# Kernel optimization log

Measured on AMD Instinct MI355X. Metric: run time of the kernel, lower is better.

The kernel has to match this reference:

```python
import jax, jax.numpy as jnp
import numpy as np

TOPK = 15
SIGMA = 2.0
VAR = (0.1, 0.2)


def point_form(p):  # cxcywh -> xyxy
    return jnp.concatenate([p[..., :2] - p[..., 2:] / 2, p[..., :2] + p[..., 2:] / 2], -1)


def decode(loc, priors):  # loc [P,4], priors cxcywh [P,4] -> xyxy
    xy = priors[:, :2] + loc[:, :2] * VAR[0] * priors[:, 2:]
    wh = priors[:, 2:] * jnp.exp(loc[:, 2:] * VAR[1])
    return jnp.concatenate([xy - wh / 2, xy + wh / 2], -1)


def encode(matched, priors):  # matched xyxy [...,4], priors cxcywh [...,4]
    g_cxcy = ((matched[..., :2] + matched[..., 2:]) / 2 - priors[..., :2]) / (VAR[0] * priors[..., 2:])
    g_wh = jnp.log((matched[..., 2:] - matched[..., :2]) / priors[..., 2:]) / VAR[1]
    return jnp.concatenate([g_cxcy, g_wh], -1)


def jaccard(a, b):  # a [O,4], b [P,4] xyxy -> [O,P]
    lt = jnp.maximum(a[:, None, :2], b[None, :, :2])
    rb = jnp.minimum(a[:, None, 2:], b[None, :, 2:])
    wh = jnp.clip(rb - lt, 0.0)
    inter = wh[..., 0] * wh[..., 1]
    area_a = (a[:, 2] - a[:, 0]) * (a[:, 3] - a[:, 1])
    area_b = (b[:, 2] - b[:, 0]) * (b[:, 3] - b[:, 1])
    return inter / (area_a[:, None] + area_b[None, :] - inter)


def boost_topk(mat):
    # per object row: num_pos = max(1, int(sum of top-15 scores)); add 3.0 to top num_pos anchors
    vals, idxs = jax.lax.top_k(mat, TOPK)                       # [O,TOPK]
    num_pos = jnp.maximum(1, vals.sum(axis=1).astype(jnp.int32))  # trunc like .int()
    add = jnp.where(jnp.arange(TOPK)[None, :] < num_pos[:, None], 3.0, 0.0)
    return jax.vmap(lambda row, i, a: row.at[i].add(a))(mat, idxs, add)


def mutual_match(truths, labels, regress, classif, priors):
    reg_ov = jaccard(truths, decode(regress, priors))           # [O,P]
    reg_ov = jnp.where(reg_ov == reg_ov.max(0, keepdims=True), reg_ov, 0.0)
    reg_ov = boost_topk(reg_ov)
    overlap_t = reg_ov.max(0)
    conf_t = labels[jnp.argmax(reg_ov, 0)] + 1
    ov = jaccard(truths, point_form(priors))                    # [O,P]
    pc = jax.nn.sigmoid(classif)[:, labels].T                   # [O,P]
    pred = ov ** ((SIGMA - pc) / SIGMA)
    pred = jnp.where(pred == pred.max(0, keepdims=True), pred, 0.0)
    pred = boost_topk(pred)
    pred_t = pred.max(0)
    loc_t = truths[jnp.argmax(pred, 0)]
    return loc_t, conf_t, overlap_t, pred_t


def balanced_l1(pred, target, alpha=0.5, gamma=1.5, beta=0.11):
    diff = jnp.abs(pred - target)
    b = np.float32(np.e ** (gamma / alpha) - 1.0)
    small = alpha / b * (b * diff + 1.0) * jnp.log1p(b * diff / beta) - alpha * diff
    big = gamma * diff + gamma / b - alpha * beta
    return jnp.where(diff < beta, small, big)


def gfocal_loss(logits, targets, gamma=2.0):
    # quality focal loss with soft IoU targets
    bce = jnp.maximum(logits, 0.0) - logits * targets + jnp.log1p(jnp.exp(-jnp.abs(logits)))
    scale = jnp.abs(jax.nn.sigmoid(logits) - targets) ** gamma
    num_pos = jnp.maximum((targets > 0).sum().astype(logits.dtype), 1.0)
    return (scale * bce).sum() / num_pos


def setup_inputs() -> dict:
    key = jax.random.key(0)
    k1, k2, k3, k4, k5, k6 = jax.random.split(key, 6)
    N, P, C, O = 32, 18000, 80, 16
    loc_data = jax.random.normal(k1, (N, P, 4), jnp.float32)
    conf_data = jax.random.normal(k2, (N, P, C), jnp.float32)
    pc = jax.random.uniform(k3, (P, 2), minval=0.05, maxval=0.95)
    pwh = jax.random.uniform(k4, (P, 2), minval=0.02, maxval=0.3)
    priors = jnp.concatenate([pc, pwh], -1)                     # cxcywh
    tc = jax.random.uniform(k5, (N, O, 2), minval=0.2, maxval=0.8)
    twh = jax.random.uniform(jax.random.fold_in(k5, 1), (N, O, 2), minval=0.05, maxval=0.4)
    truths = jnp.clip(jnp.concatenate([tc - twh / 2, tc + twh / 2], -1), 0.0, 1.0)  # xyxy
    labels = jax.random.randint(k6, (N, O), 0, C)
    return {"loc_data": loc_data, "conf_data": conf_data, "priors": priors,
            "truths": truths, "labels": labels}


def reference(loc_data, conf_data, priors, truths, labels):
    loc_t, conf_t, overlap_t, pred_t = jax.vmap(
        lambda t, l, r, c: mutual_match(t, l, r, c, priors)
    )(truths, labels, loc_data, conf_data)
    loc_t = jax.lax.stop_gradient(loc_t)          # matching done under no_grad
    overlap_t = jax.lax.stop_gradient(overlap_t)
    pred_t = jax.lax.stop_gradient(pred_t)

    # localization: weighted balanced L1 over positives (pred_t >= 3 -> weight relu(pred_t-3))
    w = jnp.broadcast_to(jax.nn.relu(pred_t - 3.0)[..., None], loc_data.shape)
    w = w / w.sum()
    pri = jnp.broadcast_to(priors[None], loc_data.shape)
    target = jax.lax.stop_gradient(encode(loc_t, pri))
    loss_l = (balanced_l1(loc_data, target) * w).sum()

    # classification: soft one-hot targets weighted by relu(overlap_t-3)
    num_classes = conf_data.shape[-1]
    conf_tz = jnp.where(overlap_t <= 1.0, 0, conf_t)
    batch_label = jax.nn.one_hot(conf_tz, num_classes + 1, dtype=conf_data.dtype)[..., 1:]
    batch_label = batch_label * jax.nn.relu(overlap_t - 3.0)[..., None]
    batch_label = jax.lax.stop_gradient(batch_label)
    loss_c = gfocal_loss(conf_data, batch_label)
    return loss_l, loss_c
```

## Files before the change

### kernel.cpp

```cpp
#include <hip/hip_runtime.h>
#include <hip/hip_bf16.h>

typedef unsigned long long u64;
typedef unsigned int u32;

#define LOG2E 1.44269504088896340736f
#define LN2   0.69314718055994530942f
#define CAP   768

__device__ __forceinline__ float fexp2(float x) { return __builtin_amdgcn_exp2f(x); }
__device__ __forceinline__ float flog2(float x) { return __builtin_amdgcn_logf(x); }
__device__ __forceinline__ float frcp(float x)  { return __builtin_amdgcn_rcpf(x); }
__device__ __forceinline__ float keyval(u64 k) { return __uint_as_float((u32)(k >> 32)); }

__device__ __forceinline__ float iou_xyxy(float ax1, float ay1, float ax2, float ay2,
                                          float bx1, float by1, float bx2, float by2) {
    float ltx = fmaxf(ax1, bx1), lty = fmaxf(ay1, by1);
    float rbx = fminf(ax2, bx2), rby = fminf(ay2, by2);
    float w = fmaxf(rbx - ltx, 0.0f), h = fmaxf(rby - lty, 0.0f);
    float inter = w * h;
    float areaA = (ax2 - ax1) * (ay2 - ay1);
    float areaB = (bx2 - bx1) * (by2 - by1);
    return inter / (areaA + areaB - inter);
}

__global__ __launch_bounds__(256) void k_main(
        const float* __restrict__ loc, const float* __restrict__ conf,
        const float* __restrict__ priors, const float* __restrict__ truths,
        const int* __restrict__ labels,
        u64* __restrict__ basekeyR, u64* __restrict__ basekeyP,
        double* __restrict__ partC, u32* __restrict__ pcnt, u32* __restrict__ pcnt2,
        int P) {
    int n = blockIdx.y, p0 = blockIdx.x * 64, tid = threadIdx.x;
    int r = tid >> 2, sub = tid & 3, p = p0 + r;
    bool act = p < P;

    if (blockIdx.x == 0 && tid == 0) { pcnt[n] = 0u; pcnt2[n] = 0u; }

    float4 L0, L1, L2, L3, L4, prv, lc;
    L0 = L1 = L2 = L3 = L4 = prv = lc = make_float4(0.f, 0.f, 0.f, 0.f);
    if (act) {
        const float* rowp = conf + ((size_t)n * P + p) * 80 + sub * 4;
        L0 = *(const float4*)(rowp);
        L1 = *(const float4*)(rowp + 16);
        L2 = *(const float4*)(rowp + 32);
        L3 = *(const float4*)(rowp + 48);
        L4 = *(const float4*)(rowp + 64);
        prv = *(const float4*)(priors + (size_t)p * 4);
        lc  = *(const float4*)(loc + ((size_t)n * P + p) * 4);
    }

    __shared__ float strt[64];
    __shared__ int   lab[16];
    __shared__ u32   smask[80];
    __shared__ float sglab[64][17];
    if (tid < 64) strt[tid] = truths[n * 64 + tid];
    if (tid < 80) smask[tid] = 0u;
    __syncthreads();
    if (tid < 16) {
        int lb = labels[n * 16 + tid];
        lab[tid] = lb;
        atomicOr(&smask[lb], 1u << tid);
    }
    __syncthreads();

    u32 mybits = 0;
    #pragma unroll
    for (int k = 0; k < 5; k++) {
        #pragma unroll
        for (int j = 0; j < 4; j++) {
            if (smask[k * 16 + sub * 4 + j]) mybits |= 1u << (k * 4 + j);
        }
    }

    {
        float vv[4] = {0, 0, 0, 0};
        float vmax = 0.0f;
        if (act) {
            float cx = prv.x + lc.x * 0.1f * prv.z;
            float cy = prv.y + lc.y * 0.1f * prv.w;
            float w  = prv.z * fexp2(lc.z * 0.2f * LOG2E);
            float h  = prv.w * fexp2(lc.w * 0.2f * LOG2E);
            float bx1 = cx - w * 0.5f, by1 = cy - h * 0.5f;
            float bx2 = cx + w * 0.5f, by2 = cy + h * 0.5f;
            #pragma unroll
            for (int jj = 0; jj < 4; jj++) {
                int o = sub * 4 + jj;
                float v = iou_xyxy(strt[o * 4], strt[o * 4 + 1], strt[o * 4 + 2],
                                   strt[o * 4 + 3], bx1, by1, bx2, by2);
                vv[jj] = v;
                vmax = fmaxf(vmax, v);
            }
        }
        vmax = fmaxf(vmax, __shfl_xor(vmax, 1, 64));
        vmax = fmaxf(vmax, __shfl_xor(vmax, 2, 64));
        u32 bits = 0;
        #pragma unroll
        for (int jj = 0; jj < 4; jj++) {
            if (act && vv[jj] == vmax) bits |= 1u << (sub * 4 + jj);
        }
        bits |= __shfl_xor(bits, 1, 64);
        bits |= __shfl_xor(bits, 2, 64);
        if (act && sub == 0) {
            basekeyR[(size_t)n * P + p] = ((u64)__float_as_uint(vmax) << 32) | bits;
        }
    }

    float lsum = 0.0f;
    if (act) {
        float lv[20] = {L0.x, L0.y, L0.z, L0.w, L1.x, L1.y, L1.z, L1.w,
                        L2.x, L2.y, L2.z, L2.w, L3.x, L3.y, L3.z, L3.w,
                        L4.x, L4.y, L4.z, L4.w};
        #pragma unroll
        for (int k = 0; k < 5; k++) {
            #pragma unroll
            for (int j = 0; j < 4; j++) {
                float lg = lv[k * 4 + j];
                float e  = fexp2(-fabsf(lg) * LOG2E);
                float ln1pe = flog2(1.0f + e) * LN2;
                float rc = frcp(1.0f + e);
                float sg = (lg >= 0.0f) ? rc : e * rc;
                lsum += sg * sg * (fmaxf(lg, 0.0f) + ln1pe);
                if (mybits & (1u << (k * 4 + j))) {
                    u32 m16 = smask[k * 16 + sub * 4 + j];
                    while (m16) {
                        int o = __ffs(m16) - 1;
                        sglab[r][o] = sg;
                        m16 &= m16 - 1;
                    }
                }
            }
        }
    }
    __syncthreads();

    {
        float pv[4] = {0, 0, 0, 0};
        float pmax = 0.0f;
        if (act) {
            float px1 = prv.x - prv.z * 0.5f, py1 = prv.y - prv.w * 0.5f;
            float px2 = prv.x + prv.z * 0.5f, py2 = prv.y + prv.w * 0.5f;
            #pragma unroll
            for (int jj = 0; jj < 4; jj++) {
                int o = sub * 4 + jj;
                float ov = iou_xyxy(strt[o * 4], strt[o * 4 + 1], strt[o * 4 + 2],
                                    strt[o * 4 + 3], px1, py1, px2, py2);
                float pd = 0.0f;
                if (ov > 0.0f) {
                    float pc = sglab[r][o];
                    pd = fexp2((2.0f - pc) * 0.5f * flog2(ov));
                }
                pv[jj] = pd;
                pmax = fmaxf(pmax, pd);
            }
        }
        pmax = fmaxf(pmax, __shfl_xor(pmax, 1, 64));
        pmax = fmaxf(pmax, __shfl_xor(pmax, 2, 64));
        u32 bits = 0;
        #pragma unroll
        for (int jj = 0; jj < 4; jj++) {
            if (act && pv[jj] == pmax) bits |= 1u << (sub * 4 + jj);
        }
        bits |= __shfl_xor(bits, 1, 64);
        bits |= __shfl_xor(bits, 2, 64);
        if (act && sub == 0) {
            basekeyP[(size_t)n * P + p] = ((u64)__float_as_uint(pmax) << 32) | bits;
        }
    }

    #pragma unroll
    for (int s = 32; s > 0; s >>= 1) lsum += __shfl_down(lsum, s, 64);
    __shared__ float wsum[4];
    if ((tid & 63) == 0) wsum[tid >> 6] = lsum;
    __syncthreads();
    if (tid == 0) {
        partC[(size_t)blockIdx.y * gridDim.x + blockIdx.x] =
            (double)wsum[0] + (double)wsum[1] + (double)wsum[2] + (double)wsum[3];
    }
}

__global__ __launch_bounds__(256) void k_sel(
        const u64* __restrict__ basekeyR, const u64* __restrict__ basekeyP,
        u64* __restrict__ selk, int P, int ROWS) {
    int row = blockIdx.x, z = blockIdx.y, tid = threadIdx.x;
    int n = row >> 4, o = row & 15;
    const u64* base = (z ? basekeyP : basekeyR) + (size_t)n * P;

    __shared__ u32 hist[2048];
    __shared__ u32 tsum[256];
    __shared__ int sB;
    __shared__ u32 sSB;
    __shared__ u32 sT;
    __shared__ u64 cand[CAP];
    __shared__ u32 scnt;
    __shared__ u64 sel[15];

    if (tid == 0) scnt = 0u;
    if (tid < 15) sel[tid] = 0ULL;

    u64 pmask = 0, pval = 0;
    int shift = 53;
    int k = 0;
    int need = 15;
    bool done = false;

    for (int lvl = 0; lvl < 3 && !done; lvl++) {
        #pragma unroll
        for (int i = 0; i < 8; i++) hist[tid + i * 256] = 0u;
        __syncthreads();
        for (int i = tid * 2; i < P; i += 512) {
            ulonglong2 v = *(const ulonglong2*)(base + i);
            u64 b0 = v.x, b1 = v.y;
            if ((u32)(b0 >> 32) != 0u && ((b0 >> o) & 1) && (b0 & pmask) == pval)
                atomicAdd(&hist[(u32)(b0 >> shift) & 2047u], 1u);
            if ((u32)(b1 >> 32) != 0u && ((b1 >> o) & 1) && (b1 & pmask) == pval)
                atomicAdd(&hist[(u32)(b1 >> shift) & 2047u], 1u);
        }
        __syncthreads();
        u32 l_[8], ls[8];
        #pragma unroll
        for (int i = 0; i < 8; i++) l_[i] = hist[tid * 8 + i];
        ls[7] = l_[7];
        #pragma unroll
        for (int i = 6; i >= 0; i--) ls[i] = ls[i + 1] + l_[i];
        tsum[tid] = ls[0];
        __syncthreads();
        for (int d = 1; d < 256; d <<= 1) {
            u32 v = (tid + d < 256) ? tsum[tid + d] : 0u;
            __syncthreads();
            tsum[tid] += v;
            __syncthreads();
        }
        if (lvl == 0) {
            if (tid == 0) sT = tsum[0];
            __syncthreads();
            u32 T = sT;
            if (T == 0u) { k = 0; break; }
            k = (T < 15u) ? (int)T : 15;
            need = k;
        }
        u32 off = (tid < 255) ? tsum[tid + 1] : 0u;
        int myB = -1;
        #pragma unroll
        for (int i = 0; i < 8; i++) {
            u32 S = ls[i] + off;
            if ((int)S >= need) { int b = tid * 8 + i; if (b > myB) myB = b; }
        }
        if (tid == 0) sB = -1;
        __syncthreads();
        if (myB >= 0) atomicMax(&sB, myB);
        __syncthreads();
        int B = sB;
        if (B >= 0 && (B >> 3) == tid) sSB = ls[B & 7] + off;
        __syncthreads();
        u32 SB = sSB;
        bool last = (lvl == 2);
        bool fits = ((scnt + SB) <= (u32)CAP) || last;
        for (int i = tid * 2; i < P; i += 512) {
            ulonglong2 v = *(const ulonglong2*)(base + i);
            #pragma unroll
            for (int j = 0; j < 2; j++) {
                u64 b = (j == 0) ? v.x : v.y;
                int pp = i + j;
                if ((u32)(b >> 32) != 0u && ((b >> o) & 1) && (b & pmask) == pval) {
                    int bin = (int)((u32)(b >> shift) & 2047u);
                    bool take = fits ? (bin >= B) : (bin > B);
                    if (take) {
                        u32 idx = atomicAdd(&scnt, 1u);
                        if (idx < (u32)CAP)
                            cand[idx] = (b & 0xFFFFFFFF00000000ULL) | (u32)(~(u32)pp);
                    }
                }
            }
        }
        __syncthreads();
        if (fits) {
            done = true;
        } else {
            need = k - (int)scnt;
            pmask |= (u64)2047u << shift;
            pval |= ((u64)(u32)B) << shift;
            shift -= 11;
            __syncthreads();
        }
    }

    __syncthreads();
    if (k > 0) {
        u32 cnt = scnt; if (cnt > (u32)CAP) cnt = (u32)CAP;
        for (u32 i = tid; i < cnt; i += 256) {
            u64 key = cand[i];
            int rank = 0;
            for (u32 c = 0; c < cnt; c++) rank += (cand[c] > key) ? 1 : 0;
            if (rank < k) sel[rank] = key;
        }
    }
    __syncthreads();
    if (tid < 15) selk[((size_t)z * ROWS + row) * 16 + tid] = sel[tid];
}

__global__ __launch_bounds__(64) void k_boost(
        const u64* __restrict__ selk,
        u64* __restrict__ basekeyR, u64* __restrict__ basekeyP,
        u32* __restrict__ plistP, u64* __restrict__ plistE, u32* __restrict__ pcnt,
        u32* __restrict__ plistP2, u64* __restrict__ plistE2, u32* __restrict__ pcnt2,
        int P, int ROWS) {
    int row = blockIdx.x, z = blockIdx.y, tid = threadIdx.x;
    int n = row >> 4, o = row & 15;
    u64* bkey = z ? basekeyP : basekeyR;
    u32* lp = z ? plistP2 : plistP;
    u64* le = z ? plistE2 : plistE;
    u32* lc = z ? pcnt2 : pcnt;
    const u64* src = selk + ((size_t)z * ROWS + row) * 16;

    __shared__ int sh_num;
    if (tid == 0) {
        float s = 0.0f; int pc = 0;
        #pragma unroll
        for (int j = 0; j < 15; j++) {
            float v = keyval(src[j]);
            s += v;
            if (v > 0.0f) pc++;
        }
        int np = (int)s; if (np < 1) np = 1;
        if (pc == 0) {
            u64 bk = ((u64)__float_as_uint(3.0f) << 32) | (u32)(~(u32)o);
            atomicMax(&bkey[(size_t)n * P + 0], bk);
            u32 idx = atomicAdd(&lc[n], 1u);
            lp[n * 256 + idx] = 0u;
            le[n * 256 + idx] = bk;
            sh_num = 0;
        } else {
            sh_num = np;
        }
    }
    __syncthreads();
    if (tid < 15 && tid < sh_num) {
        u64 kx = src[tid];
        float v = keyval(kx);
        if (v > 0.0f) {
            u32 pidx = ~(u32)(kx & 0xFFFFFFFFULL);
            u64 bk = ((u64)__float_as_uint(v + 3.0f) << 32) | (u32)(~(u32)o);
            atomicMax(&bkey[(size_t)n * P + pidx], bk);
            u32 idx = atomicAdd(&lc[n], 1u);
            lp[n * 256 + idx] = pidx;
            le[n * 256 + idx] = bk;
        }
    }
}

__global__ __launch_bounds__(256) void k_tail(
        const float* __restrict__ conf, const float* __restrict__ loc,
        const float* __restrict__ priors, const float* __restrict__ truths,
        const int* __restrict__ labels,
        const u64* __restrict__ bkeyR, const u64* __restrict__ bkeyP,
        const u32* __restrict__ plistP, const u64* __restrict__ plistE,
        const u32* __restrict__ pcnt,
        const u32* __restrict__ plistP2, const u64* __restrict__ plistE2,
        const u32* __restrict__ pcnt2,
        double* __restrict__ partCC, u32* __restrict__ posCnt,
        double* __restrict__ partL, double* __restrict__ partR, int P) {
    int n = blockIdx.x, tid = threadIdx.x;
    __shared__ int lab[16];
    __shared__ float strt[64];
    if (tid < 16) lab[tid] = labels[n * 16 + tid];
    if (tid < 64) strt[tid] = truths[n * 64 + tid];
    __syncthreads();

    int cnt = (int)pcnt[n];
    float dsum = 0.0f;
    int mypos = 0;
    for (int t = tid; t < cnt; t += 256) {
        u32 p = plistP[n * 256 + t];
        u64 bk = plistE[n * 256 + t];
        u64 kx = bkeyR[(size_t)n * P + p];
        if (kx == bk) {
            float v3 = keyval(kx);
            float vt = v3 - 3.0f;
            if (vt > 0.0f) {
                mypos++;
                int o = (int)(~(u32)(kx & 0xFFFFFFFFULL)) & 15;
                int tcls = lab[o];
                float lg = conf[((size_t)n * P + p) * 80 + tcls];
                float e  = fexp2(-fabsf(lg) * LOG2E);
                float ln1pe = flog2(1.0f + e) * LN2;
                float rc = frcp(1.0f + e);
                float sg = (lg >= 0.0f) ? rc : e * rc;
                float bce0 = fmaxf(lg, 0.0f) + ln1pe;
                float bce1 = fmaxf(lg, 0.0f) - lg * vt + ln1pe;
                float d1 = sg - vt;
                dsum += d1 * d1 * bce1 - sg * sg * bce0;
            }
        }
    }

    int cnt2 = (int)pcnt2[n];
    float rsum = 0.0f, csum = 0.0f;
    for (int t = tid; t < cnt2; t += 256) {
        u32 p = plistP2[n * 256 + t];
        u64 bk = plistE2[n * 256 + t];
        u64 kx = bkeyP[(size_t)n * P + p];
        if (kx == bk) {
            float pt = keyval(kx);
            float r = pt - 3.0f;
            if (r > 0.0f) {
                int best = (int)(~(u32)(kx & 0xFFFFFFFFULL)) & 15;
                const float Bc   = (float)19.085536923187668;
                const float beta = 0.11f;
                float4 pr = *(const float4*)(priors + (size_t)p * 4);
                float tx1 = strt[best * 4],     ty1 = strt[best * 4 + 1];
                float tx2 = strt[best * 4 + 2], ty2 = strt[best * 4 + 3];
                float gcx = ((tx1 + tx2) * 0.5f - pr.x) / (0.1f * pr.z);
                float gcy = ((ty1 + ty2) * 0.5f - pr.y) / (0.1f * pr.w);
                float gw  = flog2((tx2 - tx1) / pr.z) * LN2 / 0.2f;
                float gh  = flog2((ty2 - ty1) / pr.w) * LN2 / 0.2f;
                float4 l  = *(const float4*)(loc + ((size_t)n * P + p) * 4);
                float tgt[4] = {gcx, gcy, gw, gh};
                float lvv[4] = {l.x, l.y, l.z, l.w};
                float s = 0.0f;
                #pragma unroll
                for (int j = 0; j < 4; j++) {
                    float diff = fabsf(lvv[j] - tgt[j]);
                    float bl;
                    if (diff < beta) {
                        bl = 0.5f / Bc * (Bc * diff + 1.0f) *
                             (flog2(1.0f + Bc * diff / beta) * LN2) - 0.5f * diff;
                    } else {
                        bl = 1.5f * diff + 1.5f / Bc - 0.5f * beta;
                    }
                    s += bl;
                }
                rsum += r;
                csum += r * s;
            }
        }
    }

    double dd = (double)dsum, dl = (double)csum, dr = (double)rsum;
    long long pp = mypos;
    #pragma unroll
    for (int s = 32; s > 0; s >>= 1) {
        dd += __shfl_down(dd, s, 64);
        dl += __shfl_down(dl, s, 64);
        dr += __shfl_down(dr, s, 64);
        pp += __shfl_down(pp, s, 64);
    }
    __shared__ double wd[4], wl[4], wr[4];
    __shared__ long long wp[4];
    int wv = tid >> 6;
    if ((tid & 63) == 0) { wd[wv] = dd; wl[wv] = dl; wr[wv] = dr; wp[wv] = pp; }
    __syncthreads();
    if (tid == 0) {
        partCC[n] = wd[0] + wd[1] + wd[2] + wd[3];
        partL[n]  = wl[0] + wl[1] + wl[2] + wl[3];
        partR[n]  = wr[0] + wr[1] + wr[2] + wr[3];
        posCnt[n] = (u32)(wp[0] + wp[1] + wp[2] + wp[3]);
    }
}

__global__ __launch_bounds__(256) void k_fin(
        const double* __restrict__ partC, int nC, const double* __restrict__ partCC,
        const double* __restrict__ partL, const double* __restrict__ partR,
        const u32* __restrict__ posCnt, int N, float* __restrict__ out) {
    int tid = threadIdx.x;
    double sC = 0, sL = 0, sR = 0;
    long long pos = 0;
    for (int i = tid; i < nC; i += 256) sC += partC[i];
    for (int i = tid; i < N; i += 256) {
        sC += partCC[i]; sL += partL[i]; sR += partR[i];
        pos += (long long)posCnt[i];
    }
    #pragma unroll
    for (int s = 32; s > 0; s >>= 1) {
        sC += __shfl_down(sC, s, 64);
        sL += __shfl_down(sL, s, 64);
        sR += __shfl_down(sR, s, 64);
        pos += __shfl_down(pos, s, 64);
    }
    __shared__ double aC[4], aL[4], aR[4];
    __shared__ long long aP[4];
    int wv = tid >> 6;
    if ((tid & 63) == 0) { aC[wv] = sC; aL[wv] = sL; aR[wv] = sR; aP[wv] = pos; }
    __syncthreads();
    if (tid == 0) {
        double tC = aC[0] + aC[1] + aC[2] + aC[3];
        double tL = aL[0] + aL[1] + aL[2] + aL[3];
        double tR = aR[0] + aR[1] + aR[2] + aR[3];
        long long tP = aP[0] + aP[1] + aP[2] + aP[3];
        double npos = tP > 0 ? (double)tP : 1.0;
        out[0] = (float)(tL / (4.0 * tR));
        out[1] = (float)(tC / npos);
    }
}

extern "C" void kernel_launch(void* const* d_in, const int* in_sizes, int n_in,
                              void* d_out, int out_size, void* d_ws, size_t ws_size,
                              hipStream_t stream) {
    const float* loc    = (const float*)d_in[0];
    const float* conf   = (const float*)d_in[1];
    const float* priors = (const float*)d_in[2];
    const float* truths = (const float*)d_in[3];
    const int*   labels = (const int*)d_in[4];

    int P = in_sizes[2] / 4;
    int N = in_sizes[0] / (P * 4);
    int NBLK = (P + 63) / 64;
    int ROWS = N * 16;
    int nC = NBLK * N;

    char* cur = (char*)d_ws;
    auto alloc = [&](size_t bytes) { char* r = cur; cur += (bytes + 255) & ~(size_t)255; return r; };
    u32* pcnt      = (u32*)alloc((size_t)N * 4);
    u32* pcnt2     = (u32*)alloc((size_t)N * 4);
    u32* posCnt    = (u32*)alloc((size_t)N * 4);
    double* partCC = (double*)alloc((size_t)N * 8);
    u32* plistP    = (u32*)alloc((size_t)N * 256 * 4);
    u64* plistE    = (u64*)alloc((size_t)N * 256 * 8);
    u32* plistP2   = (u32*)alloc((size_t)N * 256 * 4);
    u64* plistE2   = (u64*)alloc((size_t)N * 256 * 8);
    double* partC  = (double*)alloc((size_t)nC * 8);
    double* partL  = (double*)alloc((size_t)N * 8);
    double* partR  = (double*)alloc((size_t)N * 8);
    u64* selk      = (u64*)alloc((size_t)2 * ROWS * 16 * 8);
    u64* basekeyR  = (u64*)alloc((size_t)N * P * 8);
    u64* basekeyP  = (u64*)alloc((size_t)N * P * 8);
    float* out = (float*)d_out;

    dim3 blk(256);
    dim3 gridB(NBLK, N);
    dim3 gridS(ROWS, 2);

    k_main<<<gridB, blk, 0, stream>>>(loc, conf, priors, truths, labels,
                                      basekeyR, basekeyP, partC, pcnt, pcnt2, P);
    k_sel<<<gridS, blk, 0, stream>>>(basekeyR, basekeyP, selk, P, ROWS);
    k_boost<<<gridS, 64, 0, stream>>>(selk, basekeyR, basekeyP,
                                      plistP, plistE, pcnt,
                                      plistP2, plistE2, pcnt2, P, ROWS);
    k_tail<<<N, blk, 0, stream>>>(conf, loc, priors, truths, labels,
                                  basekeyR, basekeyP,
                                  plistP, plistE, pcnt,
                                  plistP2, plistE2, pcnt2,
                                  partCC, posCnt, partL, partR, P);
    k_fin<<<1, blk, 0, stream>>>(partC, nC, partCC, partL, partR, posCnt, N, out);
}
```

Baseline: 126.0 us.

## Single-pass top-k candidate capture in k_sel and drop shared sigmoid-by-label staging

The selection kernel now does one global scan that builds the histogram and also caches every candidate key (up to 3072) in shared memory. The top bin is then filtered from that cache, and ranks are taken over at most 256 keys. The multi-level radix rescan over global memory only runs if that fast path overflows. Separately, k_main no longer builds label masks and a shared sigmoid table with extra barriers: it reads the 4 needed logits per thread directly and recomputes the sigmoid. The trade-off is much larger shared memory in k_sel, which may cut occupancy, plus a few redundant global loads and sigmoid evaluations.

Result: slower. 128.6 us (+2.1%).

```diff
diff --git a/kernel.cpp b/kernel.cpp
--- a/kernel.cpp
+++ b/kernel.cpp
@@ -6,12 +6,18 @@
 
 #define LOG2E 1.44269504088896340736f
 #define LN2   0.69314718055994530942f
-#define CAP   768
+#define CAPA  3072
+#define CAPF  768
 
 __device__ __forceinline__ float fexp2(float x) { return __builtin_amdgcn_exp2f(x); }
 __device__ __forceinline__ float flog2(float x) { return __builtin_amdgcn_logf(x); }
 __device__ __forceinline__ float frcp(float x)  { return __builtin_amdgcn_rcpf(x); }
 __device__ __forceinline__ float keyval(u64 k) { return __uint_as_float((u32)(k >> 32)); }
+__device__ __forceinline__ float fsigmoid(float x) {
+    float e = fexp2(-fabsf(x) * LOG2E);
+    float r = frcp(1.0f + e);
+    return x >= 0.0f ? r : e * r;
+}
 
 __device__ __forceinline__ float iou_xyxy(float ax1, float ay1, float ax2, float ay2,
                                           float bx1, float by1, float bx2, float by2) {
@@ -39,38 +45,28 @@
 
     float4 L0, L1, L2, L3, L4, prv, lc;
     L0 = L1 = L2 = L3 = L4 = prv = lc = make_float4(0.f, 0.f, 0.f, 0.f);
+    const float* rowp = conf + ((size_t)n * P + p) * 80;
     if (act) {
-        const float* rowp = conf + ((size_t)n * P + p) * 80 + sub * 4;
-        L0 = *(const float4*)(rowp);
-        L1 = *(const float4*)(rowp + 16);
-        L2 = *(const float4*)(rowp + 32);
-        L3 = *(const float4*)(rowp + 48);
-        L4 = *(const float4*)(rowp + 64);
+        const float* rp = rowp + sub * 4;
+        L0 = *(const float4*)(rp);
+        L1 = *(const float4*)(rp + 16);
+        L2 = *(const float4*)(rp + 32);
+        L3 = *(const float4*)(rp + 48);
+        L4 = *(const float4*)(rp + 64);
         prv = *(const float4*)(priors + (size_t)p * 4);
         lc  = *(const float4*)(loc + ((size_t)n * P + p) * 4);
     }
 
     __shared__ float strt[64];
     __shared__ int   lab[16];
-    __shared__ u32   smask[80];
-    __shared__ float sglab[64][17];
     if (tid < 64) strt[tid] = truths[n * 64 + tid];
-    if (tid < 80) smask[tid] = 0u;
-    __syncthreads();
-    if (tid < 16) {
-        int lb = labels[n * 16 + tid];
-        lab[tid] = lb;
-        atomicOr(&smask[lb], 1u << tid);
-    }
-    __syncthreads();
-
-    u32 mybits = 0;
-    #pragma unroll
-    for (int k = 0; k < 5; k++) {
-        #pragma unroll
-        for (int j = 0; j < 4; j++) {
-            if (smask[k * 16 + sub * 4 + j]) mybits |= 1u << (k * 4 + j);
-        }
+    if (tid < 16) lab[tid] = labels[n * 16 + tid];
+    __syncthreads();
+
+    float glab[4] = {0, 0, 0, 0};
+    if (act) {
+        #pragma unroll
+        for (int jj = 0; jj < 4; jj++) glab[jj] = rowp[lab[sub * 4 + jj]];
     }
 
     {
@@ -112,27 +108,15 @@
                         L2.x, L2.y, L2.z, L2.w, L3.x, L3.y, L3.z, L3.w,
                         L4.x, L4.y, L4.z, L4.w};
         #pragma unroll
-        for (int k = 0; k < 5; k++) {
-            #pragma unroll
-            for (int j = 0; j < 4; j++) {
-                float lg = lv[k * 4 + j];
-                float e  = fexp2(-fabsf(lg) * LOG2E);
-                float ln1pe = flog2(1.0f + e) * LN2;
-                float rc = frcp(1.0f + e);
-                float sg = (lg >= 0.0f) ? rc : e * rc;
-                lsum += sg * sg * (fmaxf(lg, 0.0f) + ln1pe);
-                if (mybits & (1u << (k * 4 + j))) {
-                    u32 m16 = smask[k * 16 + sub * 4 + j];
-                    while (m16) {
-                        int o = __ffs(m16) - 1;
-                        sglab[r][o] = sg;
-                        m16 &= m16 - 1;
-                    }
-                }
-            }
-        }
-    }
-    __syncthreads();
+        for (int k = 0; k < 20; k++) {
+            float lg = lv[k];
+            float e  = fexp2(-fabsf(lg) * LOG2E);
+            float ln1pe = flog2(1.0f + e) * LN2;
+            float rc = frcp(1.0f + e);
+            float sg = (lg >= 0.0f) ? rc : e * rc;
+            lsum += sg * sg * (fmaxf(lg, 0.0f) + ln1pe);
+        }
+    }
 
     {
         float pv[4] = {0, 0, 0, 0};
@@ -147,7 +131,7 @@
                                     strt[o * 4 + 3], px1, py1, px2, py2);
                 float pd = 0.0f;
                 if (ov > 0.0f) {
-                    float pc = sglab[r][o];
+                    float pc = fsigmoid(glab[jj]);
                     pd = fexp2((2.0f - pc) * 0.5f * flog2(ov));
                 }
                 pv[jj] = pd;
@@ -191,108 +175,174 @@
     __shared__ int sB;
     __shared__ u32 sSB;
     __shared__ u32 sT;
-    __shared__ u64 cand[CAP];
+    __shared__ u64 cand[CAPA];
     __shared__ u32 scnt;
+    __shared__ u64 small_[256];
+    __shared__ u32 smcnt;
     __shared__ u64 sel[15];
-
-    if (tid == 0) scnt = 0u;
+    __shared__ int s_done;
+
+    if (tid == 0) { scnt = 0u; smcnt = 0u; s_done = 0; }
     if (tid < 15) sel[tid] = 0ULL;
-
-    u64 pmask = 0, pval = 0;
-    int shift = 53;
-    int k = 0;
-    int need = 15;
-    bool done = false;
-
-    for (int lvl = 0; lvl < 3 && !done; lvl++) {
-        #pragma unroll
-        for (int i = 0; i < 8; i++) hist[tid + i * 256] = 0u;
+    #pragma unroll
+    for (int i = 0; i < 8; i++) hist[tid + i * 256] = 0u;
+    __syncthreads();
+
+    for (int i = tid * 2; i < P; i += 512) {
+        ulonglong2 v = *(const ulonglong2*)(base + i);
+        #pragma unroll
+        for (int j = 0; j < 2; j++) {
+            u64 b = j ? v.y : v.x;
+            if ((u32)(b >> 32) != 0u && ((b >> o) & 1)) {
+                atomicAdd(&hist[(u32)(b >> 53) & 2047u], 1u);
+                u32 idx = atomicAdd(&scnt, 1u);
+                if (idx < (u32)CAPA)
+                    cand[idx] = (b & 0xFFFFFFFF00000000ULL) | (u32)(~(u32)(i + j));
+            }
+        }
+    }
+    __syncthreads();
+
+    u32 l_[8], ls[8];
+    #pragma unroll
+    for (int i = 0; i < 8; i++) l_[i] = hist[tid * 8 + i];
+    ls[7] = l_[7];
+    #pragma unroll
+    for (int i = 6; i >= 0; i--) ls[i] = ls[i + 1] + l_[i];
+    tsum[tid] = ls[0];
+    __syncthreads();
+    for (int d = 1; d < 256; d <<= 1) {
+        u32 v = (tid + d < 256) ? tsum[tid + d] : 0u;
         __syncthreads();
-        for (int i = tid * 2; i < P; i += 512) {
-            ulonglong2 v = *(const ulonglong2*)(base + i);
-            u64 b0 = v.x, b1 = v.y;
-            if ((u32)(b0 >> 32) != 0u && ((b0 >> o) & 1) && (b0 & pmask) == pval)
-                atomicAdd(&hist[(u32)(b0 >> shift) & 2047u], 1u);
-            if ((u32)(b1 >> 32) != 0u && ((b1 >> o) & 1) && (b1 & pmask) == pval)
-                atomicAdd(&hist[(u32)(b1 >> shift) & 2047u], 1u);
-        }
+        tsum[tid] += v;
         __syncthreads();
-        u32 l_[8], ls[8];
-        #pragma unroll
-        for (int i = 0; i < 8; i++) l_[i] = hist[tid * 8 + i];
-        ls[7] = l_[7];
-        #pragma unroll
-        for (int i = 6; i >= 0; i--) ls[i] = ls[i + 1] + l_[i];
-        tsum[tid] = ls[0];
-        __syncthreads();
-        for (int d = 1; d < 256; d <<= 1) {
-            u32 v = (tid + d < 256) ? tsum[tid + d] : 0u;
-            __syncthreads();
-            tsum[tid] += v;
-            __syncthreads();
-        }
-        if (lvl == 0) {
-            if (tid == 0) sT = tsum[0];
-            __syncthreads();
-            u32 T = sT;
-            if (T == 0u) { k = 0; break; }
-            k = (T < 15u) ? (int)T : 15;
-            need = k;
-        }
+    }
+    if (tid == 0) sT = tsum[0];
+    __syncthreads();
+    u32 T = sT;
+    int k = (T < 15u) ? (int)T : 15;
+    if (T != 0u) {
         u32 off = (tid < 255) ? tsum[tid + 1] : 0u;
         int myB = -1;
         #pragma unroll
         for (int i = 0; i < 8; i++) {
-            u32 S = ls[i] + off;
-            if ((int)S >= need) { int b = tid * 8 + i; if (b > myB) myB = b; }
+            if ((int)(ls[i] + off) >= k) { int b = tid * 8 + i; if (b > myB) myB = b; }
         }
         if (tid == 0) sB = -1;
         __syncthreads();
         if (myB >= 0) atomicMax(&sB, myB);
         __syncthreads();
         int B = sB;
-        if (B >= 0 && (B >> 3) == tid) sSB = ls[B & 7] + off;
-        __syncthreads();
-        u32 SB = sSB;
-        bool last = (lvl == 2);
-        bool fits = ((scnt + SB) <= (u32)CAP) || last;
-        for (int i = tid * 2; i < P; i += 512) {
-            ulonglong2 v = *(const ulonglong2*)(base + i);
-            #pragma unroll
-            for (int j = 0; j < 2; j++) {
-                u64 b = (j == 0) ? v.x : v.y;
-                int pp = i + j;
-                if ((u32)(b >> 32) != 0u && ((b >> o) & 1) && (b & pmask) == pval) {
-                    int bin = (int)((u32)(b >> shift) & 2047u);
-                    bool take = fits ? (bin >= B) : (bin > B);
-                    if (take) {
-                        u32 idx = atomicAdd(&scnt, 1u);
-                        if (idx < (u32)CAP)
-                            cand[idx] = (b & 0xFFFFFFFF00000000ULL) | (u32)(~(u32)pp);
+
+        if (scnt <= (u32)CAPA) {
+            u32 cnt = scnt;
+            for (u32 i = tid; i < cnt; i += 256) {
+                u64 key = cand[i];
+                if ((int)((u32)(key >> 53) & 2047u) >= B) {
+                    u32 idx = atomicAdd(&smcnt, 1u);
+                    if (idx < 256u) small_[idx] = key;
+                }
+            }
+            __syncthreads();
+            if (smcnt <= 256u) {
+                u32 sc = smcnt;
+                if (tid < (int)sc) {
+                    u64 key = small_[tid];
+                    int rank = 0;
+                    for (u32 c = 0; c < sc; c++) rank += (small_[c] > key) ? 1 : 0;
+                    if (rank < k) sel[rank] = key;
+                }
+                if (tid == 0) s_done = 1;
+            }
+            __syncthreads();
+        }
+
+        if (!s_done) {
+            if (tid == 0) scnt = 0u;
+            __syncthreads();
+            u64 pmask = 0, pval = 0;
+            int shift = 53;
+            int need = k;
+            bool done = false;
+            for (int lvl = 0; lvl < 3 && !done; lvl++) {
+                #pragma unroll
+                for (int i = 0; i < 8; i++) hist[tid + i * 256] = 0u;
+                __syncthreads();
+                for (int i = tid * 2; i < P; i += 512) {
+                    ulonglong2 v = *(const ulonglong2*)(base + i);
+                    #pragma unroll
+                    for (int j = 0; j < 2; j++) {
+                        u64 b = j ? v.y : v.x;
+                        if ((u32)(b >> 32) != 0u && ((b >> o) & 1) && (b & pmask) == pval)
+                            atomicAdd(&hist[(u32)(b >> shift) & 2047u], 1u);
                     }
                 }
-            }
-        }
-        __syncthreads();
-        if (fits) {
-            done = true;
-        } else {
-            need = k - (int)scnt;
-            pmask |= (u64)2047u << shift;
-            pval |= ((u64)(u32)B) << shift;
-            shift -= 11;
-            __syncthreads();
-        }
-    }
-
-    __syncthreads();
-    if (k > 0) {
-        u32 cnt = scnt; if (cnt > (u32)CAP) cnt = (u32)CAP;
-        for (u32 i = tid; i < cnt; i += 256) {
-            u64 key = cand[i];
-            int rank = 0;
-            for (u32 c = 0; c < cnt; c++) rank += (cand[c] > key) ? 1 : 0;
-            if (rank < k) sel[rank] = key;
+                __syncthreads();
+                u32 m_[8], ms[8];
+                #pragma unroll
+                for (int i = 0; i < 8; i++) m_[i] = hist[tid * 8 + i];
+                ms[7] = m_[7];
+                #pragma unroll
+                for (int i = 6; i >= 0; i--) ms[i] = ms[i + 1] + m_[i];
+                tsum[tid] = ms[0];
+                __syncthreads();
+                for (int d = 1; d < 256; d <<= 1) {
+                    u32 v = (tid + d < 256) ? tsum[tid + d] : 0u;
+                    __syncthreads();
+                    tsum[tid] += v;
+                    __syncthreads();
+                }
+                u32 off2 = (tid < 255) ? tsum[tid + 1] : 0u;
+                int myB2 = -1;
+                #pragma unroll
+                for (int i = 0; i < 8; i++) {
+                    if ((int)(ms[i] + off2) >= need) { int b = tid * 8 + i; if (b > myB2) myB2 = b; }
+                }
+                if (tid == 0) sB = -1;
+                __syncthreads();
+                if (myB2 >= 0) atomicMax(&sB, myB2);
+                __syncthreads();
+                int B2 = sB;
+                if (B2 >= 0 && (B2 >> 3) == tid) sSB = ms[B2 & 7] + off2;
+                __syncthreads();
+                u32 SB = sSB;
+                bool last = (lvl == 2);
+                bool fits = ((scnt + SB) <= (u32)CAPF) || last;
+                for (int i = tid * 2; i < P; i += 512) {
+                    ulonglong2 v = *(const ulonglong2*)(base + i);
+                    #pragma unroll
+                    for (int j = 0; j < 2; j++) {
+                        u64 b = j ? v.y : v.x;
+                        int pp = i + j;
+                        if ((u32)(b >> 32) != 0u && ((b >> o) & 1) && (b & pmask) == pval) {
+                            int bin = (int)((u32)(b >> shift) & 2047u);
+                            bool take = fits ? (bin >= B2) : (bin > B2);
+                            if (take) {
+                                u32 idx = atomicAdd(&scnt, 1u);
+                                if (idx < (u32)CAPF)
+                                    cand[idx] = (b & 0xFFFFFFFF00000000ULL) | (u32)(~(u32)pp);
+                            }
+                        }
+                    }
+                }
+                __syncthreads();
+                if (fits) {
+                    done = true;
+                } else {
+                    need = k - (int)scnt;
+                    pmask |= (u64)2047u << shift;
+                    pval |= ((u64)(u32)B2) << shift;
+                    shift -= 11;
+                    __syncthreads();
+                }
+            }
+            u32 cnt = scnt; if (cnt > (u32)CAPF) cnt = (u32)CAPF;
+            for (u32 i = tid; i < cnt; i += 256) {
+                u64 key = cand[i];
+                int rank = 0;
+                for (u32 c = 0; c < cnt; c++) rank += (cand[c] > key) ? 1 : 0;
+                if (rank < k) sel[rank] = key;
+            }
         }
     }
     __syncthreads();
```

## Fuse boost into top-k selection and resolve anchor conflicts in shared memory

Applied to the files above, without the earlier changes.

The k_boost kernel is folded into k_sel, which writes the positive-candidate lists directly from its shared selection, so one launch and the selk round trip go away. Global atomicMax updates on the per-anchor key arrays are dropped. k_tail now loads each image's candidate list into shared memory and picks the winning entry per anchor with a quadratic scan, replacing the global key lookup. This removes a launch and scattered atomics, but adds an O(cnt^2) shared-memory scan and relies on the candidate list holding every entry that could raise an anchor's key above its base value.

After: 173.3 us. +37.6%, slower.

```diff
diff --git a/kernel.cpp b/kernel.cpp
--- a/kernel.cpp
+++ b/kernel.cpp
@@ -181,7 +181,9 @@
 
 __global__ __launch_bounds__(256) void k_sel(
         const u64* __restrict__ basekeyR, const u64* __restrict__ basekeyP,
-        u64* __restrict__ selk, int P, int ROWS) {
+        u32* __restrict__ plistP, u64* __restrict__ plistE, u32* __restrict__ pcnt,
+        u32* __restrict__ plistP2, u64* __restrict__ plistE2, u32* __restrict__ pcnt2,
+        int P, int ROWS) {
     int row = blockIdx.x, z = blockIdx.y, tid = threadIdx.x;
     int n = row >> 4, o = row & 15;
     const u64* base = (z ? basekeyP : basekeyR) + (size_t)n * P;
@@ -296,55 +298,35 @@
         }
     }
     __syncthreads();
-    if (tid < 15) selk[((size_t)z * ROWS + row) * 16 + tid] = sel[tid];
-}
-
-__global__ __launch_bounds__(64) void k_boost(
-        const u64* __restrict__ selk,
-        u64* __restrict__ basekeyR, u64* __restrict__ basekeyP,
-        u32* __restrict__ plistP, u64* __restrict__ plistE, u32* __restrict__ pcnt,
-        u32* __restrict__ plistP2, u64* __restrict__ plistE2, u32* __restrict__ pcnt2,
-        int P, int ROWS) {
-    int row = blockIdx.x, z = blockIdx.y, tid = threadIdx.x;
-    int n = row >> 4, o = row & 15;
-    u64* bkey = z ? basekeyP : basekeyR;
-    u32* lp = z ? plistP2 : plistP;
-    u64* le = z ? plistE2 : plistE;
-    u32* lc = z ? pcnt2 : pcnt;
-    const u64* src = selk + ((size_t)z * ROWS + row) * 16;
-
-    __shared__ int sh_num;
+
     if (tid == 0) {
+        u32* lp = z ? plistP2 : plistP;
+        u64* le = z ? plistE2 : plistE;
+        u32* lc = z ? pcnt2 : pcnt;
         float s = 0.0f; int pc = 0;
         #pragma unroll
         for (int j = 0; j < 15; j++) {
-            float v = keyval(src[j]);
+            float v = keyval(sel[j]);
             s += v;
             if (v > 0.0f) pc++;
         }
         int np = (int)s; if (np < 1) np = 1;
         if (pc == 0) {
             u64 bk = ((u64)__float_as_uint(3.0f) << 32) | (u32)(~(u32)o);
-            atomicMax(&bkey[(size_t)n * P + 0], bk);
             u32 idx = atomicAdd(&lc[n], 1u);
             lp[n * 256 + idx] = 0u;
             le[n * 256 + idx] = bk;
-            sh_num = 0;
         } else {
-            sh_num = np;
-        }
-    }
-    __syncthreads();
-    if (tid < 15 && tid < sh_num) {
-        u64 kx = src[tid];
-        float v = keyval(kx);
-        if (v > 0.0f) {
-            u32 pidx = ~(u32)(kx & 0xFFFFFFFFULL);
-            u64 bk = ((u64)__float_as_uint(v + 3.0f) << 32) | (u32)(~(u32)o);
-            atomicMax(&bkey[(size_t)n * P + pidx], bk);
-            u32 idx = atomicAdd(&lc[n], 1u);
-            lp[n * 256 + idx] = pidx;
-            le[n * 256 + idx] = bk;
+            int m = np < pc ? np : pc;
+            for (int j = 0; j < m; j++) {
+                u64 kx = sel[j];
+                float v = keyval(kx);
+                u32 pidx = ~(u32)(kx & 0xFFFFFFFFULL);
+                u64 bk = ((u64)__float_as_uint(v + 3.0f) << 32) | (u32)(~(u32)o);
+                u32 idx = atomicAdd(&lc[n], 1u);
+                lp[n * 256 + idx] = pidx;
+                le[n * 256 + idx] = bk;
+            }
         }
     }
 }
@@ -353,7 +335,6 @@
         const float* __restrict__ conf, const float* __restrict__ loc,
         const float* __restrict__ priors, const float* __restrict__ truths,
         const int* __restrict__ labels,
-        const u64* __restrict__ bkeyR, const u64* __restrict__ bkeyP,
         const u32* __restrict__ plistP, const u64* __restrict__ plistE,
         const u32* __restrict__ pcnt,
         const u32* __restrict__ plistP2, const u64* __restrict__ plistE2,
@@ -363,23 +344,31 @@
     int n = blockIdx.x, tid = threadIdx.x;
     __shared__ int lab[16];
     __shared__ float strt[64];
+    __shared__ u32 sp[256];
+    __shared__ u64 se[256];
     if (tid < 16) lab[tid] = labels[n * 16 + tid];
     if (tid < 64) strt[tid] = truths[n * 64 + tid];
-    __syncthreads();
 
     int cnt = (int)pcnt[n];
+    for (int i = tid; i < cnt; i += 256) {
+        sp[i] = plistP[n * 256 + i];
+        se[i] = plistE[n * 256 + i];
+    }
+    __syncthreads();
     float dsum = 0.0f;
     int mypos = 0;
     for (int t = tid; t < cnt; t += 256) {
-        u32 p = plistP[n * 256 + t];
-        u64 bk = plistE[n * 256 + t];
-        u64 kx = bkeyR[(size_t)n * P + p];
-        if (kx == bk) {
-            float v3 = keyval(kx);
+        u32 p = sp[t];
+        u64 bk = se[t];
+        bool win = true;
+        for (int c = 0; c < cnt; c++)
+            if (sp[c] == p && se[c] > bk) win = false;
+        if (win) {
+            float v3 = keyval(bk);
             float vt = v3 - 3.0f;
             if (vt > 0.0f) {
                 mypos++;
-                int o = (int)(~(u32)(kx & 0xFFFFFFFFULL)) & 15;
+                int o = (int)(~(u32)(bk & 0xFFFFFFFFULL)) & 15;
                 int tcls = lab[o];
                 float lg = conf[((size_t)n * P + p) * 80 + tcls];
                 float e  = fexp2(-fabsf(lg) * LOG2E);
@@ -393,18 +382,26 @@
             }
         }
     }
+    __syncthreads();
 
     int cnt2 = (int)pcnt2[n];
+    for (int i = tid; i < cnt2; i += 256) {
+        sp[i] = plistP2[n * 256 + i];
+        se[i] = plistE2[n * 256 + i];
+    }
+    __syncthreads();
     float rsum = 0.0f, csum = 0.0f;
     for (int t = tid; t < cnt2; t += 256) {
-        u32 p = plistP2[n * 256 + t];
-        u64 bk = plistE2[n * 256 + t];
-        u64 kx = bkeyP[(size_t)n * P + p];
-        if (kx == bk) {
-            float pt = keyval(kx);
+        u32 p = sp[t];
+        u64 bk = se[t];
+        bool win = true;
+        for (int c = 0; c < cnt2; c++)
+            if (sp[c] == p && se[c] > bk) win = false;
+        if (win) {
+            float pt = keyval(bk);
             float r = pt - 3.0f;
             if (r > 0.0f) {
-                int best = (int)(~(u32)(kx & 0xFFFFFFFFULL)) & 15;
+                int best = (int)(~(u32)(bk & 0xFFFFFFFFULL)) & 15;
                 const float Bc   = (float)19.085536923187668;
                 const float beta = 0.11f;
                 float4 pr = *(const float4*)(priors + (size_t)p * 4);
@@ -521,7 +518,6 @@
     double* partC  = (double*)alloc((size_t)nC * 8);
     double* partL  = (double*)alloc((size_t)N * 8);
     double* partR  = (double*)alloc((size_t)N * 8);
-    u64* selk      = (u64*)alloc((size_t)2 * ROWS * 16 * 8);
     u64* basekeyR  = (u64*)alloc((size_t)N * P * 8);
     u64* basekeyP  = (u64*)alloc((size_t)N * P * 8);
     float* out = (float*)d_out;
@@ -532,12 +528,10 @@
 
     k_main<<<gridB, blk, 0, stream>>>(loc, conf, priors, truths, labels,
                                       basekeyR, basekeyP, partC, pcnt, pcnt2, P);
-    k_sel<<<gridS, blk, 0, stream>>>(basekeyR, basekeyP, selk, P, ROWS);
-    k_boost<<<gridS, 64, 0, stream>>>(selk, basekeyR, basekeyP,
-                                      plistP, plistE, pcnt,
-                                      plistP2, plistE2, pcnt2, P, ROWS);
+    k_sel<<<gridS, blk, 0, stream>>>(basekeyR, basekeyP,
+                                     plistP, plistE, pcnt,
+                                     plistP2, plistE2, pcnt2, P, ROWS);
     k_tail<<<N, blk, 0, stream>>>(conf, loc, priors, truths, labels,
-                                  basekeyR, basekeyP,
                                   plistP, plistE, pcnt,
                                   plistP2, plistE2, pcnt2,
                                   partCC, posCnt, partL, partR, P);
```

## Process four prior chunks per block with register double-buffered prefetch in k_main

Applied to the files above, without the earlier changes.

k_main now handles four 64-prior chunks per block instead of one, and the grid shrinks to match. Per-chunk loading and compute are split into helper functions. The next chunk's conf, prior and loc data is loaded into an alternate register set while the current chunk is computed. The goal is to hide global-load latency and spread the per-block setup (truths, labels, masks) over more work, at the cost of roughly doubled register use and fewer resident blocks.

Result: slower. 138.6 us (+10.0%).

```diff
diff --git a/kernel.cpp b/kernel.cpp
--- a/kernel.cpp
+++ b/kernel.cpp
@@ -24,22 +24,14 @@
     return inter / (areaA + areaB - inter);
 }
 
-__global__ __launch_bounds__(256) void k_main(
-        const float* __restrict__ loc, const float* __restrict__ conf,
-        const float* __restrict__ priors, const float* __restrict__ truths,
-        const int* __restrict__ labels,
-        u64* __restrict__ basekeyR, u64* __restrict__ basekeyP,
-        double* __restrict__ partC, u32* __restrict__ pcnt, u32* __restrict__ pcnt2,
-        int P) {
-    int n = blockIdx.y, p0 = blockIdx.x * 64, tid = threadIdx.x;
-    int r = tid >> 2, sub = tid & 3, p = p0 + r;
-    bool act = p < P;
-
-    if (blockIdx.x == 0 && tid == 0) { pcnt[n] = 0u; pcnt2[n] = 0u; }
-
-    float4 L0, L1, L2, L3, L4, prv, lc;
-    L0 = L1 = L2 = L3 = L4 = prv = lc = make_float4(0.f, 0.f, 0.f, 0.f);
-    if (act) {
+__device__ __forceinline__ void load_chunk(
+        int chunk, int NBLK, int P, int n, int r, int sub,
+        const float* __restrict__ conf, const float* __restrict__ priors,
+        const float* __restrict__ loc,
+        float4& L0, float4& L1, float4& L2, float4& L3, float4& L4,
+        float4& prv, float4& lcv) {
+    int p = chunk * 64 + r;
+    if (chunk < NBLK && p < P) {
         const float* rowp = conf + ((size_t)n * P + p) * 80 + sub * 4;
         L0 = *(const float4*)(rowp);
         L1 = *(const float4*)(rowp + 16);
@@ -47,40 +39,29 @@
         L3 = *(const float4*)(rowp + 48);
         L4 = *(const float4*)(rowp + 64);
         prv = *(const float4*)(priors + (size_t)p * 4);
-        lc  = *(const float4*)(loc + ((size_t)n * P + p) * 4);
-    }
-
-    __shared__ float strt[64];
-    __shared__ int   lab[16];
-    __shared__ u32   smask[80];
-    __shared__ float sglab[64][17];
-    if (tid < 64) strt[tid] = truths[n * 64 + tid];
-    if (tid < 80) smask[tid] = 0u;
-    __syncthreads();
-    if (tid < 16) {
-        int lb = labels[n * 16 + tid];
-        lab[tid] = lb;
-        atomicOr(&smask[lb], 1u << tid);
-    }
-    __syncthreads();
-
-    u32 mybits = 0;
-    #pragma unroll
-    for (int k = 0; k < 5; k++) {
-        #pragma unroll
-        for (int j = 0; j < 4; j++) {
-            if (smask[k * 16 + sub * 4 + j]) mybits |= 1u << (k * 4 + j);
-        }
-    }
+        lcv = *(const float4*)(loc + ((size_t)n * P + p) * 4);
+    }
+}
+
+__device__ __forceinline__ void compute_chunk(
+        int chunk, int NBLK, int P, int n, int r, int sub, int tid,
+        float4 L0, float4 L1, float4 L2, float4 L3, float4 L4,
+        float4 prv, float4 lcv,
+        const float* strt, const u32* smask, u32 mybits,
+        float (*sglab)[17], float* wsum,
+        u64* __restrict__ basekeyR, u64* __restrict__ basekeyP,
+        double* __restrict__ partC) {
+    int p = chunk * 64 + r;
+    bool act = (chunk < NBLK) && (p < P);
 
     {
         float vv[4] = {0, 0, 0, 0};
         float vmax = 0.0f;
         if (act) {
-            float cx = prv.x + lc.x * 0.1f * prv.z;
-            float cy = prv.y + lc.y * 0.1f * prv.w;
-            float w  = prv.z * fexp2(lc.z * 0.2f * LOG2E);
-            float h  = prv.w * fexp2(lc.w * 0.2f * LOG2E);
+            float cx = prv.x + lcv.x * 0.1f * prv.z;
+            float cy = prv.y + lcv.y * 0.1f * prv.w;
+            float w  = prv.z * fexp2(lcv.z * 0.2f * LOG2E);
+            float h  = prv.w * fexp2(lcv.w * 0.2f * LOG2E);
             float bx1 = cx - w * 0.5f, by1 = cy - h * 0.5f;
             float bx2 = cx + w * 0.5f, by2 = cy + h * 0.5f;
             #pragma unroll
@@ -170,13 +151,68 @@
 
     #pragma unroll
     for (int s = 32; s > 0; s >>= 1) lsum += __shfl_down(lsum, s, 64);
+    if ((tid & 63) == 0) wsum[tid >> 6] = lsum;
+    __syncthreads();
+    if (tid == 0 && chunk < NBLK) {
+        partC[(size_t)n * NBLK + chunk] =
+            (double)wsum[0] + (double)wsum[1] + (double)wsum[2] + (double)wsum[3];
+    }
+}
+
+__global__ __launch_bounds__(256) void k_main(
+        const float* __restrict__ loc, const float* __restrict__ conf,
+        const float* __restrict__ priors, const float* __restrict__ truths,
+        const int* __restrict__ labels,
+        u64* __restrict__ basekeyR, u64* __restrict__ basekeyP,
+        double* __restrict__ partC, u32* __restrict__ pcnt, u32* __restrict__ pcnt2,
+        int P, int NBLK) {
+    int n = blockIdx.y, tid = threadIdx.x;
+    int r = tid >> 2, sub = tid & 3;
+    int c0 = blockIdx.x * 4;
+
+    if (blockIdx.x == 0 && tid == 0) { pcnt[n] = 0u; pcnt2[n] = 0u; }
+
+    float4 A0, A1, A2, A3, A4, Ap, Al;
+    float4 B0, B1, B2, B3, B4, Bp, Bl;
+    A0 = A1 = A2 = A3 = A4 = Ap = Al = make_float4(0.f, 0.f, 0.f, 0.f);
+    B0 = B1 = B2 = B3 = B4 = Bp = Bl = make_float4(0.f, 0.f, 0.f, 0.f);
+    load_chunk(c0,     NBLK, P, n, r, sub, conf, priors, loc, A0, A1, A2, A3, A4, Ap, Al);
+    load_chunk(c0 + 1, NBLK, P, n, r, sub, conf, priors, loc, B0, B1, B2, B3, B4, Bp, Bl);
+
+    __shared__ float strt[64];
+    __shared__ int   lab[16];
+    __shared__ u32   smask[80];
+    __shared__ float sglab[64][17];
     __shared__ float wsum[4];
-    if ((tid & 63) == 0) wsum[tid >> 6] = lsum;
-    __syncthreads();
-    if (tid == 0) {
-        partC[(size_t)blockIdx.y * gridDim.x + blockIdx.x] =
-            (double)wsum[0] + (double)wsum[1] + (double)wsum[2] + (double)wsum[3];
-    }
+    if (tid < 64) strt[tid] = truths[n * 64 + tid];
+    if (tid < 80) smask[tid] = 0u;
+    __syncthreads();
+    if (tid < 16) {
+        int lb = labels[n * 16 + tid];
+        lab[tid] = lb;
+        atomicOr(&smask[lb], 1u << tid);
+    }
+    __syncthreads();
+
+    u32 mybits = 0;
+    #pragma unroll
+    for (int k = 0; k < 5; k++) {
+        #pragma unroll
+        for (int j = 0; j < 4; j++) {
+            if (smask[k * 16 + sub * 4 + j]) mybits |= 1u << (k * 4 + j);
+        }
+    }
+
+    compute_chunk(c0, NBLK, P, n, r, sub, tid, A0, A1, A2, A3, A4, Ap, Al,
+                  strt, smask, mybits, sglab, wsum, basekeyR, basekeyP, partC);
+    load_chunk(c0 + 2, NBLK, P, n, r, sub, conf, priors, loc, A0, A1, A2, A3, A4, Ap, Al);
+    compute_chunk(c0 + 1, NBLK, P, n, r, sub, tid, B0, B1, B2, B3, B4, Bp, Bl,
+                  strt, smask, mybits, sglab, wsum, basekeyR, basekeyP, partC);
+    load_chunk(c0 + 3, NBLK, P, n, r, sub, conf, priors, loc, B0, B1, B2, B3, B4, Bp, Bl);
+    compute_chunk(c0 + 2, NBLK, P, n, r, sub, tid, A0, A1, A2, A3, A4, Ap, Al,
+                  strt, smask, mybits, sglab, wsum, basekeyR, basekeyP, partC);
+    compute_chunk(c0 + 3, NBLK, P, n, r, sub, tid, B0, B1, B2, B3, B4, Bp, Bl,
+                  strt, smask, mybits, sglab, wsum, basekeyR, basekeyP, partC);
 }
 
 __global__ __launch_bounds__(256) void k_sel(
@@ -527,11 +563,11 @@
     float* out = (float*)d_out;
 
     dim3 blk(256);
-    dim3 gridB(NBLK, N);
+    dim3 gridB((NBLK + 3) / 4, N);
     dim3 gridS(ROWS, 2);
 
     k_main<<<gridB, blk, 0, stream>>>(loc, conf, priors, truths, labels,
-                                      basekeyR, basekeyP, partC, pcnt, pcnt2, P);
+                                      basekeyR, basekeyP, partC, pcnt, pcnt2, P, NBLK);
     k_sel<<<gridS, blk, 0, stream>>>(basekeyR, basekeyP, selk, P, ROWS);
     k_boost<<<gridS, 64, 0, stream>>>(selk, basekeyR, basekeyP,
                                       plistP, plistE, pcnt,
```
